# Performance work log

Hardware: AMD Instinct MI355X
Metric: run time of the kernel (lower is better)

Reference implementation:

```python
import jax, jax.numpy as jnp
import numpy as np

B, T, D, N, K, H = 2, 2048, 2560, 8, 4, 256
G = N // K
WINDOW = 1024
ROPE_BASE = 10000
K_MASK = -2.3819763e+38
EPS = 1e-6


def apply_rope(inputs, positions, base_frequency):
    # inputs: [B, L, n, H]; positions: [B, L]
    head_dim = inputs.shape[-1]
    fraction = 2 * jnp.arange(0, head_dim // 2) / head_dim
    timescale = base_frequency ** fraction
    sinusoid = positions[..., None] / timescale[None, None, :]   # [B, L, H/2]
    sinusoid = sinusoid[..., None, :]                            # [B, L, 1, H/2]
    sin, cos = jnp.sin(sinusoid), jnp.cos(sinusoid)
    first, second = jnp.split(inputs, 2, axis=-1)
    out = jnp.concatenate([first * cos - second * sin,
                           second * cos + first * sin], axis=-1)
    return out.astype(inputs.dtype)


def rms_norm(x, scale):
    # Gemma-style RMSNorm: normalize over last dim, (1 + scale) gain.
    var = jnp.mean(jnp.square(x), axis=-1, keepdims=True)
    return x * jax.lax.rsqrt(var + EPS) * (1.0 + scale)


def setup_inputs() -> dict:
    key = jax.random.key(0)
    ks = jax.random.split(key, 5)
    x = jax.random.normal(ks[0], (B, T, D), jnp.float32)
    positions = jnp.broadcast_to(jnp.arange(T, dtype=jnp.int32), (B, T))
    # Causal sliding-window mask (LOCAL_SLIDING, window=1024), shape [B, 1, T, S].
    qp = jnp.arange(T)[:, None]
    kp = jnp.arange(T)[None, :]
    mask = (kp <= qp) & ((qp - kp) < WINDOW)
    attn_mask = jnp.broadcast_to(mask[None, None], (B, 1, T, T))
    q_w = jax.random.normal(ks[1], (N, D, H), jnp.float32) * 0.02
    kv_w = jax.random.normal(ks[2], (2, K, D, H), jnp.float32) * 0.02
    q_scale = jnp.zeros((H,), jnp.float32)
    k_scale = jnp.zeros((H,), jnp.float32)
    out_w = jax.random.normal(ks[3], (N, H, D), jnp.float32) * 0.02
    return {"x": x, "q_w": q_w, "kv_w": kv_w, "q_scale": q_scale,
            "k_scale": k_scale, "out_w": out_w,
            "positions": positions, "attn_mask": attn_mask}


def reference(x, q_w, kv_w, q_scale, k_scale, out_w, positions, attn_mask):
    dtype = x.dtype
    # GQA projections (num_kv_heads != num_heads branch)
    q = jnp.einsum('BTD,NDH->BTNH', x, q_w)          # [B,T,N,H]
    k = jnp.einsum('BSD,KDH->BSKH', x, kv_w[0])      # [B,S,K,H]
    v = jnp.einsum('BSD,KDH->BSKH', x, kv_w[1])      # [B,S,K,H]
    # QK-RMSNorm (GQA branch only)
    q = rms_norm(q, q_scale)
    k = rms_norm(k, k_scale)
    # RoPE + query scaling
    q = apply_rope(q, positions, ROPE_BASE)
    q = q * (H ** -0.5)
    k = apply_rope(k, positions, ROPE_BASE)
    # Grouped attention logits: [B,T,K,G,S] -> [B,T,N,S]
    qg = q.reshape(B, T, K, G, H)
    logits = jnp.einsum('BTKGH,BSKH->BTKGS', qg, k)
    logits = logits.reshape(B, T, N, T)
    # Mask + softmax (mask [B,1,T,S] -> [B,T,1,S])
    bmask = jnp.expand_dims(attn_mask.squeeze(axis=1), axis=2)
    masked = jnp.where(bmask, logits, K_MASK)
    probs = jax.nn.softmax(masked, axis=-1).astype(dtype)
    # Weighted values with grouped kv heads
    pg = probs.reshape(B, T, K, G, T)
    enc = jnp.einsum('BTKGS,BSKH->BTKGH', pg, v).reshape(B, T, N, H)
    out = jnp.einsum('BTNH,NHD->BTD', enc, out_w)
    return out
```

## Files before the change

kernel.cpp:

```cpp
#include <hip/hip_runtime.h>
#include <cstdint>

#define TB 2048
#define DIM 2560
#define NQ 8
#define NKV 4
#define HDIM 256
#define WIN 1024
#define KMASK -2.3819763e+38f

using f32x4 = __attribute__((ext_vector_type(4))) float;
using s16x8 = __attribute__((ext_vector_type(8))) short;
using u16x4 = __attribute__((ext_vector_type(4))) unsigned short;

__device__ __forceinline__ unsigned short f2bf(float f) {
  uint32_t x = __builtin_bit_cast(uint32_t, f);
  x += 0x7FFFu + ((x >> 16) & 1u);
  return (unsigned short)(x >> 16);
}

__global__ __launch_bounds__(256) void k_packw1(const float* __restrict__ q_w,
                                                const float* __restrict__ kv_w,
                                                unsigned short* __restrict__ W1) {
  __shared__ float tile[32][33];
  const int hd = blockIdx.z;
  const float* src = (hd < 8) ? (q_w + (size_t)hd * DIM * HDIM)
                              : (kv_w + (size_t)(hd - 8) * DIM * HDIM);
  unsigned short* dst = W1 + (size_t)hd * HDIM * DIM;
  const int c0 = blockIdx.x * 32, r0 = blockIdx.y * 32;
  const int tx = threadIdx.x & 31, ty = threadIdx.x >> 5;
#pragma unroll
  for (int i = 0; i < 32; i += 8)
    tile[ty + i][tx] = src[(size_t)(r0 + ty + i) * HDIM + c0 + tx];
  __syncthreads();
#pragma unroll
  for (int i = 0; i < 32; i += 8)
    dst[(size_t)(c0 + ty + i) * DIM + r0 + tx] = f2bf(tile[tx][ty + i]);
}

__global__ __launch_bounds__(256) void k_tconv(const float* __restrict__ src,
                                               unsigned short* __restrict__ dst,
                                               int R, int C) {
  __shared__ float tile[32][33];
  const int c0 = blockIdx.x * 32, r0 = blockIdx.y * 32;
  const int tx = threadIdx.x & 31, ty = threadIdx.x >> 5;
#pragma unroll
  for (int i = 0; i < 32; i += 8)
    tile[ty + i][tx] = src[(size_t)(r0 + ty + i) * C + c0 + tx];
  __syncthreads();
#pragma unroll
  for (int i = 0; i < 32; i += 8)
    dst[(size_t)(c0 + ty + i) * R + r0 + tx] = f2bf(tile[tx][ty + i]);
}

__global__ __launch_bounds__(256) void k_cvt(const float* __restrict__ src,
                                             unsigned short* __restrict__ dst, int n4) {
  int i = blockIdx.x * 256 + threadIdx.x;
  if (i < n4) {
    f32x4 v = *(const f32x4*)&src[(size_t)i * 4];
    u16x4 o;
#pragma unroll
    for (int j = 0; j < 4; ++j) o[j] = f2bf(v[j]);
    *(u16x4*)&dst[(size_t)i * 4] = o;
  }
}

__global__ __launch_bounds__(512, 2) void k_gemm(const unsigned short* __restrict__ A,
                                                 const unsigned short* __restrict__ Bw,
                                                 float* __restrict__ Cc,
                                                 int Nc, int Kd, int nxl) {
  __shared__ unsigned short shA[2][256 * 64];
  __shared__ unsigned short shB[2][256 * 64];
  const int tid = threadIdx.x, w = tid >> 6, l = tid & 63;
  const int xcd = blockIdx.x & 7, loc = blockIdx.x >> 3;
  const int m0 = ((xcd >> 1) * 4 + loc / nxl) * 256;
  const int n0 = ((xcd & 1) * nxl + loc % nxl) * 256;

  const int srow = l >> 3;
  const int sw_colb = (((l & 7) ^ srow) << 4);
  const int wrow = w * 8;
  const int NT = Kd >> 6;

#define STG_A(buf, t, r)                                                                     \
  {                                                                                          \
    const char* src_ = (const char*)A +                                                      \
        ((size_t)(m0 + (r) * 64 + wrow + srow) * Kd + ((size_t)(t) << 6)) * 2 + sw_colb;     \
    __builtin_amdgcn_global_load_lds(                                                        \
        (__attribute__((address_space(1))) void*)src_,                                       \
        (__attribute__((address_space(3))) void*)((char*)&shA[buf][0] + (r) * 8192 + w * 1024), \
        16, 0, 0);                                                                           \
  }
#define STG_B(buf, t, r)                                                                     \
  {                                                                                          \
    const char* src_ = (const char*)Bw +                                                     \
        ((size_t)(n0 + (r) * 64 + wrow + srow) * Kd + ((size_t)(t) << 6)) * 2 + sw_colb;     \
    __builtin_amdgcn_global_load_lds(                                                        \
        (__attribute__((address_space(1))) void*)src_,                                       \
        (__attribute__((address_space(3))) void*)((char*)&shB[buf][0] + (r) * 8192 + w * 1024), \
        16, 0, 0);                                                                           \
  }

  const int wm = w >> 2, wn = w & 3;
  const int lr = l & 15, lg = l >> 4;
  const int rswz = (lr & 7) << 4;
  const int c0x = (lg * 16) ^ rswz;
  const int c1x = (64 + lg * 16) ^ rswz;
  f32x4 acc[8][4] = {};

#pragma unroll
  for (int r = 0; r < 4; ++r) { STG_A(0, 0, r); STG_B(0, 0, r); }
  asm volatile("s_waitcnt vmcnt(0)" ::: "memory");
  __builtin_amdgcn_s_barrier();

  for (int t = 0; t < NT; ++t) {
    const int buf = t & 1;
    const bool pf = (t + 1 < NT);
    const char* sa = (const char*)&shA[buf][0];
    const char* sb = (const char*)&shB[buf][0];
    s16x8 af[4], bf0[4], bf1[4];

#pragma unroll
    for (int mi = 0; mi < 4; ++mi)
      af[mi] = *(const s16x8*)(sa + (wm * 128 + mi * 16 + lr) * 128 + c0x);
#pragma unroll
    for (int ni = 0; ni < 4; ++ni)
      bf0[ni] = *(const s16x8*)(sb + (wn * 64 + ni * 16 + lr) * 128 + c0x);
    if (pf) { STG_A(buf ^ 1, t + 1, 0); STG_A(buf ^ 1, t + 1, 1); }
    __builtin_amdgcn_s_barrier();
    asm volatile("s_waitcnt lgkmcnt(0)" ::: "memory");
    __builtin_amdgcn_s_setprio(1);
#pragma unroll
    for (int mi = 0; mi < 4; ++mi)
#pragma unroll
      for (int ni = 0; ni < 4; ++ni)
        acc[mi][ni] = __builtin_amdgcn_mfma_f32_16x16x32_bf16(af[mi], bf0[ni], acc[mi][ni], 0, 0, 0);
    __builtin_amdgcn_s_setprio(0);
    __builtin_amdgcn_s_barrier();

#pragma unroll
    for (int mi = 0; mi < 4; ++mi)
      af[mi] = *(const s16x8*)(sa + (wm * 128 + (4 + mi) * 16 + lr) * 128 + c0x);
    if (pf) { STG_A(buf ^ 1, t + 1, 2); STG_A(buf ^ 1, t + 1, 3); }
    __builtin_amdgcn_s_barrier();
    asm volatile("s_waitcnt lgkmcnt(0)" ::: "memory");
    __builtin_amdgcn_s_setprio(1);
#pragma unroll
    for (int mi = 0; mi < 4; ++mi)
#pragma unroll
      for (int ni = 0; ni < 4; ++ni)
        acc[4 + mi][ni] = __builtin_amdgcn_mfma_f32_16x16x32_bf16(af[mi], bf0[ni], acc[4 + mi][ni], 0, 0, 0);
    __builtin_amdgcn_s_setprio(0);
    __builtin_amdgcn_s_barrier();

#pragma unroll
    for (int mi = 0; mi < 4; ++mi)
      af[mi] = *(const s16x8*)(sa + (wm * 128 + mi * 16 + lr) * 128 + c1x);
#pragma unroll
    for (int ni = 0; ni < 4; ++ni)
      bf1[ni] = *(const s16x8*)(sb + (wn * 64 + ni * 16 + lr) * 128 + c1x);
    if (pf) { STG_B(buf ^ 1, t + 1, 0); STG_B(buf ^ 1, t + 1, 1); }
    __builtin_amdgcn_s_barrier();
    asm volatile("s_waitcnt lgkmcnt(0)" ::: "memory");
    __builtin_amdgcn_s_setprio(1);
#pragma unroll
    for (int mi = 0; mi < 4; ++mi)
#pragma unroll
      for (int ni = 0; ni < 4; ++ni)
        acc[mi][ni] = __builtin_amdgcn_mfma_f32_16x16x32_bf16(af[mi], bf1[ni], acc[mi][ni], 0, 0, 0);
    __builtin_amdgcn_s_setprio(0);
    __builtin_amdgcn_s_barrier();

#pragma unroll
    for (int mi = 0; mi < 4; ++mi)
      af[mi] = *(const s16x8*)(sa + (wm * 128 + (4 + mi) * 16 + lr) * 128 + c1x);
    if (pf) { STG_B(buf ^ 1, t + 1, 2); STG_B(buf ^ 1, t + 1, 3); }
    __builtin_amdgcn_s_barrier();
    asm volatile("s_waitcnt lgkmcnt(0)" ::: "memory");
    __builtin_amdgcn_s_setprio(1);
#pragma unroll
    for (int mi = 0; mi < 4; ++mi)
#pragma unroll
      for (int ni = 0; ni < 4; ++ni)
        acc[4 + mi][ni] = __builtin_amdgcn_mfma_f32_16x16x32_bf16(af[mi], bf1[ni], acc[4 + mi][ni], 0, 0, 0);
    __builtin_amdgcn_s_setprio(0);
    asm volatile("s_waitcnt vmcnt(0)" ::: "memory");
    __builtin_amdgcn_s_barrier();
  }
#undef STG_A
#undef STG_B

#pragma unroll
  for (int mi = 0; mi < 8; ++mi)
#pragma unroll
    for (int ni = 0; ni < 4; ++ni) {
      size_t base = (size_t)(m0 + wm * 128 + mi * 16 + lg * 4) * Nc + (n0 + wn * 64 + ni * 16 + lr);
#pragma unroll
      for (int i = 0; i < 4; ++i)
        Cc[base + (size_t)i * Nc] = acc[mi][ni][i];
    }
}

__global__ __launch_bounds__(256) void k_normrope(const float* __restrict__ Y,
                                                  const float* __restrict__ qsc,
                                                  const float* __restrict__ ksc,
                                                  const int* __restrict__ pos,
                                                  unsigned short* __restrict__ Q,
                                                  unsigned short* __restrict__ Kb) {
  __shared__ float s_sin[128], s_cos[128];
  const int bt = blockIdx.x;
  const int b = bt >> 11, t = bt & (TB - 1);
  const int tid = threadIdx.x;
  float p = (float)pos[bt];
  if (tid < 128) {
    float fr = (float)tid * (1.0f / 128.0f);
    float inv_ts = __expf(fr * -9.210340371976184f);
    float ang = p * inv_ts;
    float sv, cv;
    sincosf(ang, &sv, &cv);
    s_sin[tid] = sv;
    s_cos[tid] = cv;
  }
  __syncthreads();
  const int w = tid >> 6, l = tid & 63;
  const int jj0 = (l & 31) * 4;
  for (int sidx = w; sidx < 12; sidx += 4) {
    const float* src = Y + (size_t)bt * 4096 + sidx * 256;
    f32x4 v = *(const f32x4*)&src[l * 4];
    float ss = v[0] * v[0] + v[1] * v[1] + v[2] * v[2] + v[3] * v[3];
#pragma unroll
    for (int d = 1; d < 64; d <<= 1) ss += __shfl_xor(ss, d);
    float rs = rsqrtf(ss * (1.0f / 256.0f) + 1e-6f);
    const float* scp = (sidx < 8) ? qsc : ksc;
    float nv[4], res[4];
#pragma unroll
    for (int j = 0; j < 4; ++j) nv[j] = v[j] * rs * (1.0f + scp[l * 4 + j]);
#pragma unroll
    for (int j = 0; j < 4; ++j) {
      float o = __shfl_xor(nv[j], 32);
      float sn = s_sin[jj0 + j], cs = s_cos[jj0 + j];
      res[j] = (l < 32) ? (nv[j] * cs - o * sn) : (nv[j] * cs + o * sn);
    }
    float qs = (sidx < 8) ? 0.0625f : 1.0f;
    u16x4 ob;
#pragma unroll
    for (int j = 0; j < 4; ++j) ob[j] = f2bf(res[j] * qs);
    if (sidx < 8) {
      size_t di = ((size_t)(b * NQ + sidx) * TB + t) * HDIM + l * 4;
      *(u16x4*)&Q[di] = ob;
    } else {
      size_t di = ((size_t)(b * NKV + (sidx - 8)) * TB + t) * HDIM + l * 4;
      *(u16x4*)&Kb[di] = ob;
    }
  }
}

__global__ __launch_bounds__(256) void k_vtrans(const float* __restrict__ Y,
                                                unsigned short* __restrict__ VT) {
  __shared__ float tile[64][65];
  const int t0 = blockIdx.x * 64, h0 = blockIdx.y * 64;
  const int z = blockIdx.z;
  const int bq = z >> 2, kh = z & 3;
  const int tid = threadIdx.x;
#pragma unroll
  for (int rep = 0; rep < 16; ++rep) {
    int idx = rep * 256 + tid;
    int tr = idx >> 6, hc = idx & 63;
    tile[tr][hc] = Y[(size_t)(bq * TB + t0 + tr) * 4096 + 3072 + kh * 256 + h0 + hc];
  }
  __syncthreads();
#pragma unroll
  for (int rep = 0; rep < 16; ++rep) {
    int idx = rep * 256 + tid;
    int hr = idx >> 6, tc = idx & 63;
    VT[((size_t)z * 256 + h0 + hr) * TB + t0 + tc] = f2bf(tile[tc][hr]);
  }
}

__global__ __launch_bounds__(256, 2) void k_attn(const unsigned short* __restrict__ Q,
                                                 const unsigned short* __restrict__ Kb,
                                                 const unsigned short* __restrict__ VT,
                                                 unsigned short* __restrict__ ENC) {
  __shared__ unsigned short shK[2][32 * 256];
  __shared__ unsigned short shV[2][256 * 32];
  __shared__ unsigned short Pb[4][16 * 40];
  const int tid = threadIdx.x, w = tid >> 6, l = tid & 63;
  const int bn = blockIdx.y;
  const int b = bn >> 3, n = bn & 7, kh = n >> 1;
  const int t0b = blockIdx.x * 64;
  const int t0 = t0b + w * 16;
  const int lr = l & 15, lg = l >> 4;
  const unsigned short* qp = Q + ((size_t)bn * TB + t0) * HDIM;
  const char* kbase = (const char*)(Kb + ((size_t)(b * NKV + kh) * TB) * HDIM);
  const char* vbase = (const char*)(VT + ((size_t)(b * NKV + kh) * HDIM) * TB);

  s16x8 aq[8];
#pragma unroll
  for (int kk = 0; kk < 8; ++kk)
    aq[kk] = *(const s16x8*)&qp[lr * HDIM + kk * 32 + lg * 8];

  f32x4 o[16] = {};
  float mrow[4], lsum[4];
#pragma unroll
  for (int i = 0; i < 4; ++i) { mrow[i] = -__builtin_inff(); lsum[i] = 0.f; }

  int lo = t0b - (WIN - 1);
  if (lo < 0) lo = 0;
  lo &= ~31;
  const int nsteps = (t0b + 32 - lo) / 32 + 1;

  const int k_row = (w << 1) + (l >> 5);
  const int k_colb = (l & 31) * 16;
  const int v_row = (w << 4) + (l >> 2);
  const int v_colb = (l & 3) * 16;
#define STAGE(buf, s0)                                                                       \
  {                                                                                          \
    _Pragma("unroll") for (int r = 0; r < 4; ++r) {                                          \
      int row = r * 8 + k_row;                                                               \
      int scol = k_colb ^ ((row & 7) << 4);                                                  \
      const char* src = kbase + (size_t)((s0) + row) * 512 + scol;                           \
      __builtin_amdgcn_global_load_lds(                                                      \
          (__attribute__((address_space(1))) void*)src,                                      \
          (__attribute__((address_space(3))) void*)((char*)&shK[buf][0] + r * 4096 + w * 1024), \
          16, 0, 0);                                                                         \
    }                                                                                        \
    _Pragma("unroll") for (int r = 0; r < 4; ++r) {                                          \
      int row = r * 64 + v_row;                                                              \
      const char* src = vbase + (size_t)row * (TB * 2) + (size_t)(s0) * 2 + v_colb;          \
      __builtin_amdgcn_global_load_lds(                                                      \
          (__attribute__((address_space(1))) void*)src,                                      \
          (__attribute__((address_space(3))) void*)((char*)&shV[buf][0] + r * 4096 + w * 1024), \
          16, 0, 0);                                                                         \
    }                                                                                        \
  }

  STAGE(0, lo);

  for (int step = 0; step < nsteps; ++step) {
    const int s0 = lo + step * 32;
    const int buf = step & 1;
    if (step + 1 < nsteps) {
      STAGE(buf ^ 1, s0 + 32);
      asm volatile("s_waitcnt vmcnt(8)" ::: "memory");
    } else {
      asm volatile("s_waitcnt vmcnt(0)" ::: "memory");
    }
    __builtin_amdgcn_s_barrier();

    const bool active = (s0 <= t0 + 15) && (s0 + 31 >= t0 - (WIN - 1));
    if (active) {
      f32x4 sacc[2] = {};
      const char* kt = (const char*)&shK[buf][0];
      const int swz = (lr & 7) << 4;
#pragma unroll
      for (int cb = 0; cb < 2; ++cb) {
        const int rb = (cb * 16 + lr) * 512;
        s16x8 bk[8];
#pragma unroll
        for (int kk = 0; kk < 8; ++kk)
          bk[kk] = *(const s16x8*)(kt + rb + ((kk * 64 + lg * 16) ^ swz));
        __builtin_amdgcn_s_setprio(1);
#pragma unroll
        for (int kk = 0; kk < 8; ++kk)
          sacc[cb] = __builtin_amdgcn_mfma_f32_16x16x32_bf16(aq[kk], bk[kk], sacc[cb], 0, 0, 0);
        __builtin_amdgcn_s_setprio(0);
      }
      float svA_[4], svB_[4];
      const bool nomask = (s0 + 31 <= t0) && (s0 >= t0 - (WIN - 16));
      if (nomask) {
#pragma unroll
        for (int i = 0; i < 4; ++i) { svA_[i] = sacc[0][i]; svB_[i] = sacc[1][i]; }
      } else {
#pragma unroll
        for (int i = 0; i < 4; ++i) {
          int trow = t0 + lg * 4 + i;
          int sA = s0 + lr, sB = s0 + 16 + lr;
          svA_[i] = ((sA <= trow) && (trow - sA < WIN)) ? sacc[0][i] : KMASK;
          svB_[i] = ((sB <= trow) && (trow - sB < WIN)) ? sacc[1][i] : KMASK;
        }
      }
      bool ok = true;
#pragma unroll
      for (int i = 0; i < 4; ++i)
        ok = ok && (svA_[i] <= mrow[i] + 8.f) && (svB_[i] <= mrow[i] + 8.f);
      if (!__all(ok)) {
        float r_[4];
#pragma unroll
        for (int i = 0; i < 4; ++i) {
          float mx = fmaxf(svA_[i], svB_[i]);
#pragma unroll
          for (int d = 1; d < 16; d <<= 1) mx = fmaxf(mx, __shfl_xor(mx, d));
          float mnew = fmaxf(mrow[i], mx);
          r_[i] = __expf(mrow[i] - mnew);
          lsum[i] *= r_[i];
          mrow[i] = mnew;
        }
#pragma unroll
        for (int hb = 0; hb < 16; ++hb)
#pragma unroll
          for (int i = 0; i < 4; ++i) o[hb][i] *= r_[i];
      }
#pragma unroll
      for (int i = 0; i < 4; ++i) {
        float pa = __expf(svA_[i] - mrow[i]);
        float pb = __expf(svB_[i] - mrow[i]);
        lsum[i] += pa + pb;
        int row = lg * 4 + i;
        Pb[w][row * 40 + lr] = f2bf(pa);
        Pb[w][row * 40 + 16 + lr] = f2bf(pb);
      }
      asm volatile("s_waitcnt lgkmcnt(0)" ::: "memory");
      s16x8 pfrag = *(const s16x8*)&Pb[w][lr * 40 + lg * 8];
      const char* vt = (const char*)&shV[buf][0];
      s16x8 vb[16];
#pragma unroll
      for (int hb = 0; hb < 16; ++hb)
        vb[hb] = *(const s16x8*)(vt + (hb * 16 + lr) * 64 + lg * 16);
      __builtin_amdgcn_s_setprio(1);
#pragma unroll
      for (int hb = 0; hb < 16; ++hb)
        o[hb] = __builtin_amdgcn_mfma_f32_16x16x32_bf16(pfrag, vb[hb], o[hb], 0, 0, 0);
      __builtin_amdgcn_s_setprio(0);
    }
    __builtin_amdgcn_s_barrier();
  }
#undef STAGE

#pragma unroll
  for (int i = 0; i < 4; ++i) {
    float s = lsum[i];
#pragma unroll
    for (int d = 1; d < 16; d <<= 1) s += __shfl_xor(s, d);
    lsum[i] = s;
  }
#pragma unroll
  for (int i = 0; i < 4; ++i) {
    int trow = t0 + lg * 4 + i;
    float inv = 1.0f / lsum[i];
    size_t rb = (size_t)(b * TB + trow) * 2048 + n * HDIM;
#pragma unroll
    for (int hb = 0; hb < 16; ++hb)
      ENC[rb + hb * 16 + lr] = f2bf(o[hb][i] * inv);
  }
}

extern "C" void kernel_launch(void* const* d_in, const int* in_sizes, int n_in,
                              void* d_out, int out_size, void* d_ws, size_t ws_size,
                              hipStream_t stream) {
  (void)in_sizes; (void)n_in; (void)out_size; (void)ws_size;
  const float* x = (const float*)d_in[0];
  const float* q_w = (const float*)d_in[1];
  const float* kv_w = (const float*)d_in[2];
  const float* qsc = (const float*)d_in[3];
  const float* ksc = (const float*)d_in[4];
  const float* out_w = (const float*)d_in[5];
  const int* pos = (const int*)d_in[6];
  float* out = (float*)d_out;

  char* ws = (char*)d_ws;
  unsigned short* W1 = (unsigned short*)(ws);
  unsigned short* W3 = (unsigned short*)(ws + 20971520);
  unsigned short* XB = (unsigned short*)(ws + 31457280);
  float* Y = (float*)(ws + 52428800);
  unsigned short* KB = (unsigned short*)(ws + 119537664);
  unsigned short* VT = (unsigned short*)(ws + 127926272);
  unsigned short* Qb = XB;
  unsigned short* ENC = (unsigned short*)(ws + 52428800);

  k_packw1<<<dim3(8, 80, 16), 256, 0, stream>>>(q_w, kv_w, W1);
  k_tconv<<<dim3(80, 64), 256, 0, stream>>>(out_w, W3, 2048, DIM);
  k_cvt<<<dim3(10240), 256, 0, stream>>>(x, XB, 2621440);
  k_gemm<<<dim3(256), 512, 0, stream>>>(XB, W1, Y, 4096, DIM, 8);
  k_normrope<<<dim3(4096), 256, 0, stream>>>(Y, qsc, ksc, pos, Qb, KB);
  k_vtrans<<<dim3(32, 4, 8), 256, 0, stream>>>(Y, VT);
  k_attn<<<dim3(32, 16), 256, 0, stream>>>(Qb, KB, VT, ENC);
  k_gemm<<<dim3(160), 512, 0, stream>>>(ENC, W3, out, DIM, 2048, 5);
}
```

Measured before the change: 260.8 us.

## Store QKV projection output as bf16 and interleave attention tile order

The first GEMM now writes its QKV projection in bf16 rather than fp32. The norm/rope and V-transpose kernels read bf16 directly, which halves the intermediate traffic to and from memory. Separately, the attention grid remaps query blocks so heavy and light causal tiles are interleaved, meant to balance load across CUs. Rounding Q/K to bf16 before RMSNorm adds a small accuracy change, and the ENC buffer is moved to a new workspace offset.

```diff
diff --git a/kernel.cpp b/kernel.cpp
--- a/kernel.cpp
+++ b/kernel.cpp
@@ -17,6 +17,11 @@
   uint32_t x = __builtin_bit_cast(uint32_t, f);
   x += 0x7FFFu + ((x >> 16) & 1u);
   return (unsigned short)(x >> 16);
+}
+
+__device__ __forceinline__ float bf2f(unsigned short u) {
+  uint32_t x = (uint32_t)u << 16;
+  return __builtin_bit_cast(float, x);
 }
 
 __global__ __launch_bounds__(256) void k_packw1(const float* __restrict__ q_w,
@@ -67,8 +72,8 @@
 
 __global__ __launch_bounds__(512, 2) void k_gemm(const unsigned short* __restrict__ A,
                                                  const unsigned short* __restrict__ Bw,
-                                                 float* __restrict__ Cc,
-                                                 int Nc, int Kd, int nxl) {
+                                                 void* __restrict__ Cc,
+                                                 int Nc, int Kd, int nxl, int bf16out) {
   __shared__ unsigned short shA[2][256 * 64];
   __shared__ unsigned short shB[2][256 * 64];
   const int tid = threadIdx.x, w = tid >> 6, l = tid & 63;
@@ -189,18 +194,32 @@
 #undef STG_A
 #undef STG_B
 
-#pragma unroll
-  for (int mi = 0; mi < 8; ++mi)
-#pragma unroll
-    for (int ni = 0; ni < 4; ++ni) {
-      size_t base = (size_t)(m0 + wm * 128 + mi * 16 + lg * 4) * Nc + (n0 + wn * 64 + ni * 16 + lr);
-#pragma unroll
-      for (int i = 0; i < 4; ++i)
-        Cc[base + (size_t)i * Nc] = acc[mi][ni][i];
-    }
-}
-
-__global__ __launch_bounds__(256) void k_normrope(const float* __restrict__ Y,
+  if (bf16out) {
+    unsigned short* Co = (unsigned short*)Cc;
+#pragma unroll
+    for (int mi = 0; mi < 8; ++mi)
+#pragma unroll
+      for (int ni = 0; ni < 4; ++ni) {
+        size_t base = (size_t)(m0 + wm * 128 + mi * 16 + lg * 4) * Nc + (n0 + wn * 64 + ni * 16 + lr);
+#pragma unroll
+        for (int i = 0; i < 4; ++i)
+          Co[base + (size_t)i * Nc] = f2bf(acc[mi][ni][i]);
+      }
+  } else {
+    float* Co = (float*)Cc;
+#pragma unroll
+    for (int mi = 0; mi < 8; ++mi)
+#pragma unroll
+      for (int ni = 0; ni < 4; ++ni) {
+        size_t base = (size_t)(m0 + wm * 128 + mi * 16 + lg * 4) * Nc + (n0 + wn * 64 + ni * 16 + lr);
+#pragma unroll
+        for (int i = 0; i < 4; ++i)
+          Co[base + (size_t)i * Nc] = acc[mi][ni][i];
+      }
+  }
+}
+
+__global__ __launch_bounds__(256) void k_normrope(const unsigned short* __restrict__ Y,
                                                   const float* __restrict__ qsc,
                                                   const float* __restrict__ ksc,
                                                   const int* __restrict__ pos,
@@ -224,8 +243,11 @@
   const int w = tid >> 6, l = tid & 63;
   const int jj0 = (l & 31) * 4;
   for (int sidx = w; sidx < 12; sidx += 4) {
-    const float* src = Y + (size_t)bt * 4096 + sidx * 256;
-    f32x4 v = *(const f32x4*)&src[l * 4];
+    const unsigned short* src = Y + (size_t)bt * 4096 + sidx * 256;
+    u16x4 vb = *(const u16x4*)&src[l * 4];
+    float v[4];
+#pragma unroll
+    for (int j = 0; j < 4; ++j) v[j] = bf2f(vb[j]);
     float ss = v[0] * v[0] + v[1] * v[1] + v[2] * v[2] + v[3] * v[3];
 #pragma unroll
     for (int d = 1; d < 64; d <<= 1) ss += __shfl_xor(ss, d);
@@ -254,9 +276,9 @@
   }
 }
 
-__global__ __launch_bounds__(256) void k_vtrans(const float* __restrict__ Y,
+__global__ __launch_bounds__(256) void k_vtrans(const unsigned short* __restrict__ Y,
                                                 unsigned short* __restrict__ VT) {
-  __shared__ float tile[64][65];
+  __shared__ unsigned short tile[64][65];
   const int t0 = blockIdx.x * 64, h0 = blockIdx.y * 64;
   const int z = blockIdx.z;
   const int bq = z >> 2, kh = z & 3;
@@ -272,7 +294,7 @@
   for (int rep = 0; rep < 16; ++rep) {
     int idx = rep * 256 + tid;
     int hr = idx >> 6, tc = idx & 63;
-    VT[((size_t)z * 256 + h0 + hr) * TB + t0 + tc] = f2bf(tile[tc][hr]);
+    VT[((size_t)z * 256 + h0 + hr) * TB + t0 + tc] = tile[tc][hr];
   }
 }
 
@@ -286,7 +308,9 @@
   const int tid = threadIdx.x, w = tid >> 6, l = tid & 63;
   const int bn = blockIdx.y;
   const int b = bn >> 3, n = bn & 7, kh = n >> 1;
-  const int t0b = blockIdx.x * 64;
+  const int xr = blockIdx.x;
+  const int xs = (xr & 1) ? (31 - (xr >> 1)) : (xr >> 1);
+  const int t0b = xs * 64;
   const int t0 = t0b + w * 16;
   const int lr = l & 15, lg = l >> 4;
   const unsigned short* qp = Q + ((size_t)bn * TB + t0) * HDIM;
@@ -460,18 +484,18 @@
   unsigned short* W1 = (unsigned short*)(ws);
   unsigned short* W3 = (unsigned short*)(ws + 20971520);
   unsigned short* XB = (unsigned short*)(ws + 31457280);
-  float* Y = (float*)(ws + 52428800);
+  unsigned short* Y = (unsigned short*)(ws + 52428800);
   unsigned short* KB = (unsigned short*)(ws + 119537664);
   unsigned short* VT = (unsigned short*)(ws + 127926272);
   unsigned short* Qb = XB;
-  unsigned short* ENC = (unsigned short*)(ws + 52428800);
+  unsigned short* ENC = (unsigned short*)(ws + 90000000);
 
   k_packw1<<<dim3(8, 80, 16), 256, 0, stream>>>(q_w, kv_w, W1);
   k_tconv<<<dim3(80, 64), 256, 0, stream>>>(out_w, W3, 2048, DIM);
   k_cvt<<<dim3(10240), 256, 0, stream>>>(x, XB, 2621440);
-  k_gemm<<<dim3(256), 512, 0, stream>>>(XB, W1, Y, 4096, DIM, 8);
+  k_gemm<<<dim3(256), 512, 0, stream>>>(XB, W1, Y, 4096, DIM, 8, 1);
   k_normrope<<<dim3(4096), 256, 0, stream>>>(Y, qsc, ksc, pos, Qb, KB);
   k_vtrans<<<dim3(32, 4, 8), 256, 0, stream>>>(Y, VT);
   k_attn<<<dim3(32, 16), 256, 0, stream>>>(Qb, KB, VT, ENC);
-  k_gemm<<<dim3(160), 512, 0, stream>>>(ENC, W3, out, DIM, 2048, 5);
-}
+  k_gemm<<<dim3(160), 512, 0, stream>>>(ENC, W3, out, DIM, 2048, 5, 0);
+}
```

Measured after the change: 255.7 us. No clear change (-1.9%).
